# Kernel optimization log

Hardware: AMD Instinct MI355X
Metric: run time of the kernel (lower is better)

## Reference

```python
import jax, jax.numpy as jnp
import numpy as np

B, N, D = 8, 256, 128
EPS = 1e-10


def setup_inputs() -> dict:
    key = jax.random.key(0)
    k1, k2, k3 = jax.random.split(key, 3)
    val_out = jax.random.normal(k1, (B, N, D), dtype=jnp.float32)
    dep_embed = jax.random.normal(k2, (B, N, N, D), dtype=jnp.float32)
    # sparse-ish binary adjacency (dependency arcs), self-loops included
    adj = (jax.random.uniform(k3, (B, N, N)) < 0.05).astype(jnp.float32)
    adj = jnp.maximum(adj, jnp.eye(N, dtype=jnp.float32)[None])
    return {"val_out": val_out, "dep_embed": dep_embed, "adj": adj}


def reference(val_out, dep_embed, adj):
    # Original builds val_cat = concat([tile(val), dep], -1) [B,N,N,2D] and computes
    # sum(val_cat * transpose(val_cat, (0,2,1,3)), -1). Algebraically this is:
    #   score[b,i,j] = <val[b,i], val[b,j]> + <dep[b,i,j], dep[b,j,i]>
    d = val_out.shape[-1]
    score = jnp.einsum('bid,bjd->bij', val_out, val_out)
    score = score + jnp.einsum('bijd,bjid->bij', dep_embed, dep_embed)
    score = score / jnp.sqrt(jnp.asarray(d, dtype=val_out.dtype))
    # adjacency-masked exp-normalize (NOT max-stabilized, to match tf.math.exp)
    exp_score = jnp.exp(score) * adj
    denom = jnp.sum(exp_score, axis=-1, keepdims=True) + EPS
    return exp_score / denom
```

## Files before the change

kernel.cpp:

```cpp
#include <hip/hip_runtime.h>
#include <math.h>


#define BB 8
#define NN 256
#define DD 128

constexpr float EPS = 1e-10f;
constexpr float INV_SQRT_D = 0.08838834764831845f;

constexpr int RECT_H = NN / 2;
constexpr int RECT_W = NN + 1;
constexpr int PAIRS_PER_BATCH = RECT_H * RECT_W;
constexpr int TOTAL_PAIRS = BB * PAIRS_PER_BATCH;
constexpr int PAIRS_PER_BLOCK = 8;

__global__ __launch_bounds__(256) void score_kernel(
    const float* __restrict__ val,
    const float* __restrict__ dep,
    const float* __restrict__ adj,
    float* __restrict__ out)
{
    const int pair = blockIdx.x * PAIRS_PER_BLOCK + (threadIdx.x >> 5);
    const int lane = threadIdx.x & 31;

    const int b = pair / PAIRS_PER_BATCH;
    const int t = pair - b * PAIRS_PER_BATCH;
    const int r = t / RECT_W;
    const int c = t - r * RECT_W;
    int i, j;
    if (c < NN - r) { i = r;          j = r + c; }
    else            { i = NN - 1 - r; j = c - 1; }

    const float4* dij = (const float4*)(dep + (((size_t)b * NN + i) * NN + j) * DD);
    const float4* dji = (const float4*)(dep + (((size_t)b * NN + j) * NN + i) * DD);
    const float4* vi  = (const float4*)(val + ((size_t)b * NN + i) * DD);
    const float4* vj  = (const float4*)(val + ((size_t)b * NN + j) * DD);

    const float4 a  = dij[lane];
    const float4 bt = dji[lane];
    const float4 x  = vi[lane];
    const float4 y  = vj[lane];

    float p = a.x * bt.x + a.y * bt.y + a.z * bt.z + a.w * bt.w
            + x.x * y.x  + x.y * y.y  + x.z * y.z  + x.w * y.w;

    #pragma unroll
    for (int m = 16; m >= 1; m >>= 1) p += __shfl_xor(p, m, 64);

    if (lane == 0) {
        const float e = __expf(p * INV_SQRT_D);
        const size_t base = (size_t)b * NN * NN;
        const size_t ij = base + (size_t)i * NN + j;
        const size_t ji = base + (size_t)j * NN + i;
        out[ij] = e * adj[ij];
        out[ji] = e * adj[ji];
    }
}

__global__ __launch_bounds__(256) void norm_kernel(float* __restrict__ out)
{
    const int row = blockIdx.x;
    const int tid = threadIdx.x;
    const size_t idx = (size_t)row * NN + tid;
    const float x = out[idx];

    float s = x;
    #pragma unroll
    for (int m = 32; m >= 1; m >>= 1) s += __shfl_xor(s, m, 64);

    __shared__ float ws[4];
    __shared__ float denom_s;
    const int wid = tid >> 6;
    if ((tid & 63) == 0) ws[wid] = s;
    __syncthreads();
    if (tid == 0) denom_s = ws[0] + ws[1] + ws[2] + ws[3] + EPS;
    __syncthreads();

    out[idx] = x / denom_s;
}

extern "C" void kernel_launch(void* const* d_in, const int* in_sizes, int n_in,
                              void* d_out, int out_size, void* d_ws, size_t ws_size,
                              hipStream_t stream) {
    const float* val = (const float*)d_in[0];
    const float* dep = (const float*)d_in[1];
    const float* adj = (const float*)d_in[2];
    float* out = (float*)d_out;

    static_assert(TOTAL_PAIRS % PAIRS_PER_BLOCK == 0, "grid exact");
    score_kernel<<<TOTAL_PAIRS / PAIRS_PER_BLOCK, 256, 0, stream>>>(val, dep, adj, out);
    norm_kernel<<<BB * NN, 256, 0, stream>>>(out);
}
```

Measured before the change: 362.6 us.

## Tile score kernel into 8x8 upper-triangular blocks with transposed dep staged in LDS

Replaces the per-pair work mapping with 8x8 tile pairs over the upper triangle. Each block stages the transposed dep tile (dep[j,i] rows) into shared memory with coalesced loads, then reads dep[i,j] directly from global. The aim is more regular memory access and less per-pair index overhead. Diagonal tiles compute the off-diagonal pairs twice, and the 32 KB of LDS per block may limit occupancy.

```diff
diff --git a/kernel.cpp b/kernel.cpp
--- a/kernel.cpp
+++ b/kernel.cpp
@@ -5,15 +5,14 @@
 #define BB 8
 #define NN 256
 #define DD 128
+#define T  8
+#define NT (NN / T)
+#define TP_PER_B ((NT * (NT + 1)) / 2)
+#define RH (NT / 2)
+#define RW (NT + 1)
 
 constexpr float EPS = 1e-10f;
 constexpr float INV_SQRT_D = 0.08838834764831845f;
-
-constexpr int RECT_H = NN / 2;
-constexpr int RECT_W = NN + 1;
-constexpr int PAIRS_PER_BATCH = RECT_H * RECT_W;
-constexpr int TOTAL_PAIRS = BB * PAIRS_PER_BATCH;
-constexpr int PAIRS_PER_BLOCK = 8;
 
 __global__ __launch_bounds__(256) void score_kernel(
     const float* __restrict__ val,
@@ -21,40 +20,60 @@
     const float* __restrict__ adj,
     float* __restrict__ out)
 {
-    const int pair = blockIdx.x * PAIRS_PER_BLOCK + (threadIdx.x >> 5);
+    __shared__ float S[T][T][DD];
+
+    const int blk = blockIdx.x;
+    const int b   = blk / TP_PER_B;
+    const int tp  = blk - b * TP_PER_B;
+    const int r   = tp / RW;
+    const int c   = tp - r * RW;
+    int ti, tj;
+    if (c < NT - r) { ti = r;          tj = r + c; }
+    else            { ti = NT - 1 - r; tj = c - 1; }
+    const int I0 = ti * T, J0 = tj * T;
+
+    {
+        const int tid = threadIdx.x;
+        #pragma unroll
+        for (int k = 0; k < 8; ++k) {
+            const int idx = k * 256 + tid;
+            const int jj  = idx >> 8;
+            const int ii  = (idx >> 5) & 7;
+            const int l   = idx & 31;
+            const float4* src = (const float4*)(dep
+                + (((size_t)b * NN + (J0 + jj)) * NN + (I0 + ii)) * DD) + l;
+            ((float4*)S)[idx] = *src;
+        }
+    }
+    __syncthreads();
+
+    const int hw   = threadIdx.x >> 5;
     const int lane = threadIdx.x & 31;
 
-    const int b = pair / PAIRS_PER_BATCH;
-    const int t = pair - b * PAIRS_PER_BATCH;
-    const int r = t / RECT_W;
-    const int c = t - r * RECT_W;
-    int i, j;
-    if (c < NN - r) { i = r;          j = r + c; }
-    else            { i = NN - 1 - r; j = c - 1; }
+    #pragma unroll
+    for (int it = 0; it < 8; ++it) {
+        const int i = I0 + it;
+        const int j = J0 + hw;
 
-    const float4* dij = (const float4*)(dep + (((size_t)b * NN + i) * NN + j) * DD);
-    const float4* dji = (const float4*)(dep + (((size_t)b * NN + j) * NN + i) * DD);
-    const float4* vi  = (const float4*)(val + ((size_t)b * NN + i) * DD);
-    const float4* vj  = (const float4*)(val + ((size_t)b * NN + j) * DD);
+        const float4 a = ((const float4*)(dep + (((size_t)b * NN + i) * NN + j) * DD))[lane];
+        const float4 t = ((const float4*)&S[hw][it][0])[lane];
+        const float4 x = ((const float4*)(val + ((size_t)b * NN + i) * DD))[lane];
+        const float4 y = ((const float4*)(val + ((size_t)b * NN + j) * DD))[lane];
 
-    const float4 a  = dij[lane];
-    const float4 bt = dji[lane];
-    const float4 x  = vi[lane];
-    const float4 y  = vj[lane];
+        float p = a.x * t.x + a.y * t.y + a.z * t.z + a.w * t.w
+                + x.x * y.x + x.y * y.y + x.z * y.z + x.w * y.w;
 
-    float p = a.x * bt.x + a.y * bt.y + a.z * bt.z + a.w * bt.w
-            + x.x * y.x  + x.y * y.y  + x.z * y.z  + x.w * y.w;
+        #pragma unroll
+        for (int m = 16; m >= 1; m >>= 1) p += __shfl_xor(p, m, 64);
 
-    #pragma unroll
-    for (int m = 16; m >= 1; m >>= 1) p += __shfl_xor(p, m, 64);
-
-    if (lane == 0) {
-        const float e = __expf(p * INV_SQRT_D);
-        const size_t base = (size_t)b * NN * NN;
-        const size_t ij = base + (size_t)i * NN + j;
-        const size_t ji = base + (size_t)j * NN + i;
-        out[ij] = e * adj[ij];
-        out[ji] = e * adj[ji];
+        if (lane == 0) {
+            const float e = __expf(p * INV_SQRT_D);
+            const size_t base = (size_t)b * NN * NN;
+            const size_t ij = base + (size_t)i * NN + j;
+            const size_t ji = base + (size_t)j * NN + i;
+            out[ij] = e * adj[ij];
+            out[ji] = e * adj[ji];
+        }
     }
 }
 
@@ -88,7 +107,6 @@
     const float* adj = (const float*)d_in[2];
     float* out = (float*)d_out;
 
-    static_assert(TOTAL_PAIRS % PAIRS_PER_BLOCK == 0, "grid exact");
-    score_kernel<<<TOTAL_PAIRS / PAIRS_PER_BLOCK, 256, 0, stream>>>(val, dep, adj, out);
+    score_kernel<<<BB * TP_PER_B, 256, 0, stream>>>(val, dep, adj, out);
     norm_kernel<<<BB * NN, 256, 0, stream>>>(out);
 }
```

Measured after the change: 377.7 us. 4.2% more time.

## Compact active adjacency pairs and gather dep only for nonzero entries

Applied to the files above, without the earlier changes.

Adds a scan kernel that reads the adjacency for each symmetric (i,j) pair, writes zeros for inactive pairs, and compacts active pair indices into a workspace list via ballot and atomic counters. A gather kernel then computes dot products only for listed pairs, avoiding reads of dep_embed rows whose output is masked to zero. This cuts most of the dominant memory traffic, at the cost of extra kernel launches, an atomic counter, and a grid sized for the worst case with early-exiting blocks.

```diff
diff --git a/kernel.cpp b/kernel.cpp
--- a/kernel.cpp
+++ b/kernel.cpp
@@ -13,48 +13,100 @@
 constexpr int RECT_W = NN + 1;
 constexpr int PAIRS_PER_BATCH = RECT_H * RECT_W;
 constexpr int TOTAL_PAIRS = BB * PAIRS_PER_BATCH;
-constexpr int PAIRS_PER_BLOCK = 8;
 
-__global__ __launch_bounds__(256) void score_kernel(
-    const float* __restrict__ val,
-    const float* __restrict__ dep,
-    const float* __restrict__ adj,
-    float* __restrict__ out)
-{
-    const int pair = blockIdx.x * PAIRS_PER_BLOCK + (threadIdx.x >> 5);
-    const int lane = threadIdx.x & 31;
-
-    const int b = pair / PAIRS_PER_BATCH;
+__device__ __forceinline__ void decode_pair(int pair, int& b, int& i, int& j) {
+    b = pair / PAIRS_PER_BATCH;
     const int t = pair - b * PAIRS_PER_BATCH;
     const int r = t / RECT_W;
     const int c = t - r * RECT_W;
-    int i, j;
     if (c < NN - r) { i = r;          j = r + c; }
     else            { i = NN - 1 - r; j = c - 1; }
+}
 
-    const float4* dij = (const float4*)(dep + (((size_t)b * NN + i) * NN + j) * DD);
-    const float4* dji = (const float4*)(dep + (((size_t)b * NN + j) * NN + i) * DD);
-    const float4* vi  = (const float4*)(val + ((size_t)b * NN + i) * DD);
-    const float4* vj  = (const float4*)(val + ((size_t)b * NN + j) * DD);
+__global__ void init_kernel(unsigned int* cnt) {
+    if (threadIdx.x == 0) *cnt = 0u;
+}
 
-    const float4 a  = dij[lane];
-    const float4 bt = dji[lane];
-    const float4 x  = vi[lane];
-    const float4 y  = vj[lane];
+__global__ __launch_bounds__(256) void scan_kernel(
+    const float* __restrict__ adj, float* __restrict__ out,
+    unsigned int* __restrict__ cnt, int* __restrict__ list)
+{
+    const int pair = blockIdx.x * 256 + threadIdx.x;
+    int b, i, j;
+    decode_pair(pair, b, i, j);
+    const size_t base = (size_t)b * NN * NN;
+    const size_t ij = base + (size_t)i * NN + j;
+    const size_t ji = base + (size_t)j * NN + i;
+    const float aij = adj[ij];
+    const float aji = adj[ji];
+    const bool active = (aij != 0.0f) || (aji != 0.0f);
+    if (!active) { out[ij] = 0.0f; out[ji] = 0.0f; }
 
-    float p = a.x * bt.x + a.y * bt.y + a.z * bt.z + a.w * bt.w
-            + x.x * y.x  + x.y * y.y  + x.z * y.z  + x.w * y.w;
+    const unsigned long long m = __ballot(active);
+    const int lane = threadIdx.x & 63;
+    const int wid  = threadIdx.x >> 6;
+    __shared__ unsigned int wcnt[4];
+    __shared__ unsigned int wbase[4];
+    if (lane == 0) wcnt[wid] = (unsigned int)__popcll(m);
+    __syncthreads();
+    if (threadIdx.x == 0) {
+        const unsigned int tot = wcnt[0] + wcnt[1] + wcnt[2] + wcnt[3];
+        const unsigned int b0 = tot ? atomicAdd(cnt, tot) : 0u;
+        wbase[0] = b0;
+        wbase[1] = b0 + wcnt[0];
+        wbase[2] = b0 + wcnt[0] + wcnt[1];
+        wbase[3] = b0 + wcnt[0] + wcnt[1] + wcnt[2];
+    }
+    __syncthreads();
+    if (active) {
+        const unsigned long long below = m & ((1ull << lane) - 1ull);
+        list[wbase[wid] + (unsigned int)__popcll(below)] = pair;
+    }
+}
+
+constexpr int B_ITERS = 8;
+constexpr int B_PAIRS_PER_BLOCK = 8 * B_ITERS;
+constexpr int B_GRID = TOTAL_PAIRS / B_PAIRS_PER_BLOCK;
+
+__global__ __launch_bounds__(256) void gather_kernel(
+    const float* __restrict__ val, const float* __restrict__ dep,
+    const float* __restrict__ adj, const unsigned int* __restrict__ cnt,
+    const int* __restrict__ list, float* __restrict__ out)
+{
+    const unsigned int n = *cnt;
+    const unsigned int base_idx = blockIdx.x * B_PAIRS_PER_BLOCK;
+    if (base_idx >= n) return;
+
+    const int hw   = threadIdx.x >> 5;
+    const int lane = threadIdx.x & 31;
 
     #pragma unroll
-    for (int m = 16; m >= 1; m >>= 1) p += __shfl_xor(p, m, 64);
-
-    if (lane == 0) {
-        const float e = __expf(p * INV_SQRT_D);
+    for (int it = 0; it < B_ITERS; ++it) {
+        const unsigned int idx = base_idx + it * 8 + hw;
+        if (idx >= n) continue;
+        const int pair = list[idx];
+        int b, i, j;
+        decode_pair(pair, b, i, j);
         const size_t base = (size_t)b * NN * NN;
         const size_t ij = base + (size_t)i * NN + j;
         const size_t ji = base + (size_t)j * NN + i;
-        out[ij] = e * adj[ij];
-        out[ji] = e * adj[ji];
+
+        const float4 a  = ((const float4*)(dep + ij * DD))[lane];
+        const float4 bt = ((const float4*)(dep + ji * DD))[lane];
+        const float4 x  = ((const float4*)(val + ((size_t)b * NN + i) * DD))[lane];
+        const float4 y  = ((const float4*)(val + ((size_t)b * NN + j) * DD))[lane];
+
+        float p = a.x * bt.x + a.y * bt.y + a.z * bt.z + a.w * bt.w
+                + x.x * y.x  + x.y * y.y  + x.z * y.z  + x.w * y.w;
+
+        #pragma unroll
+        for (int mk = 16; mk >= 1; mk >>= 1) p += __shfl_xor(p, mk, 64);
+
+        if (lane == 0) {
+            const float e = __expf(p * INV_SQRT_D);
+            out[ij] = e * adj[ij];
+            out[ji] = e * adj[ji];
+        }
     }
 }
 
@@ -88,7 +140,12 @@
     const float* adj = (const float*)d_in[2];
     float* out = (float*)d_out;
 
-    static_assert(TOTAL_PAIRS % PAIRS_PER_BLOCK == 0, "grid exact");
-    score_kernel<<<TOTAL_PAIRS / PAIRS_PER_BLOCK, 256, 0, stream>>>(val, dep, adj, out);
+    unsigned int* cnt = (unsigned int*)d_ws;
+    int* list = (int*)((char*)d_ws + 16);
+
+    static_assert(TOTAL_PAIRS % 256 == 0, "scan grid exact");
+    init_kernel<<<1, 64, 0, stream>>>(cnt);
+    scan_kernel<<<TOTAL_PAIRS / 256, 256, 0, stream>>>(adj, out, cnt, list);
+    gather_kernel<<<B_GRID, 256, 0, stream>>>(val, dep, adj, cnt, list, out);
     norm_kernel<<<BB * NN, 256, 0, stream>>>(out);
 }
```

New measurement: 334.1 us. 7.9% less time.

## Compute scores only for adjacency-active pairs in a fused per-row kernel

Applied to the files above, without the earlier changes.

Replaces the all-pairs score kernel and separate normalize kernel with one kernel per row. Each row kernel compacts the nonzero adjacency entries into a shared list and computes dot products only for those pairs. Skipping pairs whose output is masked to zero avoids reading most of the large dep tensor. The normalization is fused into the same kernel. In exchange it loses the symmetric pair sharing (dep[i,j] and dep[j,i] are both read per active entry) and assumes exp(score)*0 is zero, which fails for inf or NaN scores.

```diff
diff --git a/kernel.cpp b/kernel.cpp
--- a/kernel.cpp
+++ b/kernel.cpp
@@ -9,75 +9,76 @@
 constexpr float EPS = 1e-10f;
 constexpr float INV_SQRT_D = 0.08838834764831845f;
 
-constexpr int RECT_H = NN / 2;
-constexpr int RECT_W = NN + 1;
-constexpr int PAIRS_PER_BATCH = RECT_H * RECT_W;
-constexpr int TOTAL_PAIRS = BB * PAIRS_PER_BATCH;
-constexpr int PAIRS_PER_BLOCK = 8;
-
-__global__ __launch_bounds__(256) void score_kernel(
+__global__ __launch_bounds__(256) void row_kernel(
     const float* __restrict__ val,
     const float* __restrict__ dep,
     const float* __restrict__ adj,
     float* __restrict__ out)
 {
-    const int pair = blockIdx.x * PAIRS_PER_BLOCK + (threadIdx.x >> 5);
-    const int lane = threadIdx.x & 31;
+    const int row = blockIdx.x;
+    const int b   = row >> 8;
+    const int i   = row & 255;
+    const int tid = threadIdx.x;
 
-    const int b = pair / PAIRS_PER_BATCH;
-    const int t = pair - b * PAIRS_PER_BATCH;
-    const int r = t / RECT_W;
-    const int c = t - r * RECT_W;
-    int i, j;
-    if (c < NN - r) { i = r;          j = r + c; }
-    else            { i = NN - 1 - r; j = c - 1; }
+    __shared__ int   lst[NN];
+    __shared__ float aval[NN];
+    __shared__ float escore[NN];
+    __shared__ unsigned int wcnt[4];
+    __shared__ float wsum[4];
 
-    const float4* dij = (const float4*)(dep + (((size_t)b * NN + i) * NN + j) * DD);
-    const float4* dji = (const float4*)(dep + (((size_t)b * NN + j) * NN + i) * DD);
-    const float4* vi  = (const float4*)(val + ((size_t)b * NN + i) * DD);
-    const float4* vj  = (const float4*)(val + ((size_t)b * NN + j) * DD);
+    const float a = adj[(size_t)row * NN + tid];
+    const bool active = (a != 0.0f);
+    const unsigned long long m = __ballot(active);
+    const int lane64 = tid & 63;
+    const int wid    = tid >> 6;
+    if (lane64 == 0) wcnt[wid] = (unsigned int)__popcll(m);
+    escore[tid] = 0.0f;
+    __syncthreads();
 
-    const float4 a  = dij[lane];
-    const float4 bt = dji[lane];
-    const float4 x  = vi[lane];
-    const float4 y  = vj[lane];
+    const unsigned int n0 = wcnt[0], n1 = wcnt[1], n2 = wcnt[2], n3 = wcnt[3];
+    const int nact = (int)(n0 + n1 + n2 + n3);
+    unsigned int base = 0;
+    if (wid > 0) base += n0;
+    if (wid > 1) base += n1;
+    if (wid > 2) base += n2;
+    if (active) {
+        const unsigned long long below = m & ((1ull << lane64) - 1ull);
+        const int pos = (int)(base + (unsigned int)__popcll(below));
+        lst[pos]  = tid;
+        aval[pos] = a;
+    }
+    __syncthreads();
 
-    float p = a.x * bt.x + a.y * bt.y + a.z * bt.z + a.w * bt.w
-            + x.x * y.x  + x.y * y.y  + x.z * y.z  + x.w * y.w;
+    const int hw   = tid >> 5;
+    const int lane = tid & 31;
+    const float4 xv = ((const float4*)(val + ((size_t)b * NN + i) * DD))[lane];
 
-    #pragma unroll
-    for (int m = 16; m >= 1; m >>= 1) p += __shfl_xor(p, m, 64);
+    for (int k = hw; k < nact; k += 8) {
+        const int j = lst[k];
+        const size_t bij = (((size_t)b * NN + i) * NN + j) * DD;
+        const size_t bji = (((size_t)b * NN + j) * NN + i) * DD;
+        const float4 a4 = ((const float4*)(dep + bij))[lane];
+        const float4 b4 = ((const float4*)(dep + bji))[lane];
+        const float4 yv = ((const float4*)(val + ((size_t)b * NN + j) * DD))[lane];
 
-    if (lane == 0) {
-        const float e = __expf(p * INV_SQRT_D);
-        const size_t base = (size_t)b * NN * NN;
-        const size_t ij = base + (size_t)i * NN + j;
-        const size_t ji = base + (size_t)j * NN + i;
-        out[ij] = e * adj[ij];
-        out[ji] = e * adj[ji];
+        float p = a4.x * b4.x + a4.y * b4.y + a4.z * b4.z + a4.w * b4.w
+                + xv.x * yv.x + xv.y * yv.y + xv.z * yv.z + xv.w * yv.w;
+
+        #pragma unroll
+        for (int mk = 16; mk >= 1; mk >>= 1) p += __shfl_xor(p, mk, 64);
+
+        if (lane == 0) escore[j] = __expf(p * INV_SQRT_D) * aval[k];
     }
-}
+    __syncthreads();
 
-__global__ __launch_bounds__(256) void norm_kernel(float* __restrict__ out)
-{
-    const int row = blockIdx.x;
-    const int tid = threadIdx.x;
-    const size_t idx = (size_t)row * NN + tid;
-    const float x = out[idx];
-
+    const float x = escore[tid];
     float s = x;
     #pragma unroll
-    for (int m = 32; m >= 1; m >>= 1) s += __shfl_xor(s, m, 64);
-
-    __shared__ float ws[4];
-    __shared__ float denom_s;
-    const int wid = tid >> 6;
-    if ((tid & 63) == 0) ws[wid] = s;
+    for (int mk = 32; mk >= 1; mk >>= 1) s += __shfl_xor(s, mk, 64);
+    if (lane64 == 0) wsum[wid] = s;
     __syncthreads();
-    if (tid == 0) denom_s = ws[0] + ws[1] + ws[2] + ws[3] + EPS;
-    __syncthreads();
-
-    out[idx] = x / denom_s;
+    const float denom = wsum[0] + wsum[1] + wsum[2] + wsum[3] + EPS;
+    out[(size_t)row * NN + tid] = x / denom;
 }
 
 extern "C" void kernel_launch(void* const* d_in, const int* in_sizes, int n_in,
@@ -88,7 +89,5 @@
     const float* adj = (const float*)d_in[2];
     float* out = (float*)d_out;
 
-    static_assert(TOTAL_PAIRS % PAIRS_PER_BLOCK == 0, "grid exact");
-    score_kernel<<<TOTAL_PAIRS / PAIRS_PER_BLOCK, 256, 0, stream>>>(val, dep, adj, out);
-    norm_kernel<<<BB * NN, 256, 0, stream>>>(out);
+    row_kernel<<<BB * NN, 256, 0, stream>>>(val, dep, adj, out);
 }
```

New measurement: 306.6 us. -15.5%, faster.
